# Kernel optimization log

Hardware: AMD Instinct MI355X
Metric: run time of the kernel (lower is better)

The kernel has to match this reference:

```python
import jax, jax.numpy as jnp
import numpy as np


def setup_inputs() -> dict:
    key = jax.random.key(0)
    k1, k2 = jax.random.split(key)
    input_tensor = jax.random.normal(k1, (32, 128, 64, 64), dtype=jnp.float32)
    weights = jax.random.normal(k2, (256, 128, 3, 3), dtype=jnp.float32) * 0.05
    return {"input_tensor": input_tensor, "weights": weights}


def reference(input_tensor, weights):
    # Valid-padding, stride-1, no-bias direct conv2d (NCHW x OIHW -> NCHW),
    # identical math to the quintuple-loop slice*weight sum in the original.
    return jax.lax.conv_general_dilated(
        input_tensor,
        weights,
        window_strides=(1, 1),
        padding="VALID",
        dimension_numbers=("NCHW", "OIHW", "NCHW"),
    )
```

## Files before the change

kernel.cpp:

```cpp
#include <hip/hip_runtime.h>
#include <hip/hip_bf16.h>

#define N_IMG 32
#define CIN   128
#define INH   64
#define INW   64
#define COUT  256
#define OH    62
#define OW    62

#define IN_BLOCKS 2048
#define WT_BLOCKS (294912 / 256)

typedef short          bf16x8 __attribute__((ext_vector_type(8)));
typedef unsigned short u16x8  __attribute__((ext_vector_type(8)));
typedef float          f32x4  __attribute__((ext_vector_type(4)));
typedef float          f32x2  __attribute__((ext_vector_type(2)));

__device__ __forceinline__ unsigned short f2bf(float x) {
    unsigned int u = __float_as_uint(x);
    u += 0x7fffu + ((u >> 16) & 1u);
    return (unsigned short)(u >> 16);
}

__device__ __forceinline__ void gload_lds16(const void* g, void* l) {
    __builtin_amdgcn_global_load_lds(
        (const __attribute__((address_space(1))) unsigned int*)g,
        (__attribute__((address_space(3))) unsigned int*)l, 16, 0, 0);
}

__global__ __launch_bounds__(256)
void transform_kernel(const float* __restrict__ In,
                      const float* __restrict__ Wsrc,
                      unsigned short* __restrict__ TIn,
                      unsigned short* __restrict__ WT) {
    if (blockIdx.x >= IN_BLOCKS) {
        int idx = (blockIdx.x - IN_BLOCKS) * 256 + threadIdx.x;
        int i   = idx & 7;
        int co  = (idx >> 3) & 255;
        int cgk = idx >> 11;
        int cg  = cgk & 15;
        int khw = cgk >> 4;
        int kh  = khw / 3, kw = khw - 3 * kh;
        int ci  = cg * 8 + i;
        WT[idx] = f2bf(Wsrc[co * (CIN * 9) + ci * 9 + kh * 3 + kw]);
        return;
    }
    __shared__ float T[32][66];
    const int bid = blockIdx.x;
    const int ih0 = (bid & 15) * 4;
    const int cb  = (bid >> 4) & 3;
    const int img = bid >> 6;

    const int r   = threadIdx.x >> 3;
    const int c0  = (threadIdx.x & 7) * 8;
    const int c   = threadIdx.x;
    const int iw  = c >> 2;
    const int cg  = (c & 3) ^ ((iw >> 1) & 3);

    for (int j = 0; j < 4; ++j) {
        const int ih = ih0 + j;
        const float* p = In + (((size_t)(img * CIN + cb * 32 + r)) * INH + ih) * INW + c0;
        f32x4 a = *(const f32x4*)p;
        f32x4 b = *(const f32x4*)(p + 4);
        *(f32x2*)&T[r][c0 + 0] = f32x2{a[0], a[1]};
        *(f32x2*)&T[r][c0 + 2] = f32x2{a[2], a[3]};
        *(f32x2*)&T[r][c0 + 4] = f32x2{b[0], b[1]};
        *(f32x2*)&T[r][c0 + 6] = f32x2{b[2], b[3]};
        __syncthreads();
        u16x8 v;
#pragma unroll
        for (int i = 0; i < 8; ++i) v[i] = f2bf(T[cg * 8 + i][iw]);
        *(u16x8*)&TIn[((size_t)((img * 4 + cb) * 64 + ih) * 256 + c) * 8] = v;
        if (j < 3) __syncthreads();
    }
}

__global__ __launch_bounds__(256, 4)
void conv_mfma_bf16_kernel(const unsigned short* __restrict__ TIn,
                           const unsigned short* __restrict__ WT,
                           float* __restrict__ Out) {
    __shared__ unsigned short Lin[2][2112];

    const int g   = blockIdx.x;
    const int f   = (g & 7) * 248 + (g >> 3);
    const int img = f / OH;
    const int oh  = f - img * OH;

    const int tid  = threadIdx.x;
    const int wave = tid >> 6;
    const int lane = tid & 63;
    const int q    = lane >> 4;
    const int ml   = lane & 15;
    const int co_base = wave * 64;

    const unsigned short* tin_base = TIn + (size_t)img * (4 * 64 * 2048);
    const bf16x8* WTv = (const bf16x8*)WT;
    const int wlane = q * 256 + co_base + ml;

    int xoff[3][4];
#pragma unroll
    for (int kw = 0; kw < 3; ++kw)
#pragma unroll
        for (int ni = 0; ni < 4; ++ni) {
            const int r = ni * 16 + ml + kw;
            xoff[kw][ni] = r * 32 + ((q ^ ((r >> 1) & 3)) << 3);
        }

    f32x4 acc[4][4];
    const f32x4 zero = {0.f, 0.f, 0.f, 0.f};
#pragma unroll
    for (int a = 0; a < 4; ++a)
#pragma unroll
        for (int b = 0; b < 4; ++b) acc[a][b] = zero;

    gload_lds16(tin_base + oh * 2048 + tid * 8, &Lin[0][wave * 512]);
    if (tid < 64) ((unsigned int*)&Lin[tid >> 5][64 * 32])[tid & 31] = 0u;
    __syncthreads();

#pragma unroll
    for (int s = 0; s < 12; ++s) {
        const int cur = s & 1;
        const int kh = s >> 2, cb = s & 3;
        const bf16x8* wstage = WTv + (kh * 3 * 16 + cb * 4) * 256;

        bf16x8 wA[4], wB[4];
#pragma unroll
        for (int mi = 0; mi < 4; ++mi) wA[mi] = wstage[wlane + mi * 16];
#pragma unroll
        for (int mi = 0; mi < 4; ++mi) wB[mi] = wstage[4096 + wlane + mi * 16];

        if (s < 11) {
            const int s1 = s + 1;
            const unsigned short* src =
                tin_base + ((s1 & 3) * 64 + oh + (s1 >> 2)) * 2048;
            gload_lds16(src + tid * 8, &Lin[cur ^ 1][wave * 512]);
        }

        {
            bf16x8 xf[4];
#pragma unroll
            for (int ni = 0; ni < 4; ++ni)
                xf[ni] = *(const bf16x8*)&Lin[cur][xoff[0][ni]];
#pragma unroll
            for (int mi = 0; mi < 4; ++mi)
#pragma unroll
                for (int ni = 0; ni < 4; ++ni)
                    acc[mi][ni] = __builtin_amdgcn_mfma_f32_16x16x32_bf16(
                        wA[mi], xf[ni], acc[mi][ni], 0, 0, 0);
        }
#pragma unroll
        for (int mi = 0; mi < 4; ++mi) wA[mi] = wstage[2 * 4096 + wlane + mi * 16];
        {
            bf16x8 xf[4];
#pragma unroll
            for (int ni = 0; ni < 4; ++ni)
                xf[ni] = *(const bf16x8*)&Lin[cur][xoff[1][ni]];
#pragma unroll
            for (int mi = 0; mi < 4; ++mi)
#pragma unroll
                for (int ni = 0; ni < 4; ++ni)
                    acc[mi][ni] = __builtin_amdgcn_mfma_f32_16x16x32_bf16(
                        wB[mi], xf[ni], acc[mi][ni], 0, 0, 0);
        }
        {
            bf16x8 xf[4];
#pragma unroll
            for (int ni = 0; ni < 4; ++ni)
                xf[ni] = *(const bf16x8*)&Lin[cur][xoff[2][ni]];
#pragma unroll
            for (int mi = 0; mi < 4; ++mi)
#pragma unroll
                for (int ni = 0; ni < 4; ++ni)
                    acc[mi][ni] = __builtin_amdgcn_mfma_f32_16x16x32_bf16(
                        wA[mi], xf[ni], acc[mi][ni], 0, 0, 0);
        }
        __syncthreads();
    }

#pragma unroll
    for (int mi = 0; mi < 4; ++mi) {
#pragma unroll
        for (int r = 0; r < 4; ++r) {
            const int co = co_base + mi * 16 + q * 4 + r;
            float* op = Out + ((img * COUT + co) * OH + oh) * OW;
#pragma unroll
            for (int ni = 0; ni < 4; ++ni) {
                const int ow = ni * 16 + ml;
                if (ow < OW) op[ow] = acc[mi][ni][r];
            }
        }
    }
}

__global__ void wt_transform_kernel(const float* __restrict__ Wsrc,
                                    unsigned short* __restrict__ WT) {
    int idx = blockIdx.x * 256 + threadIdx.x;
    int i   = idx & 7;
    int co  = (idx >> 3) & 255;
    int cgk = idx >> 11;
    int cg  = cgk & 15;
    int khw = cgk >> 4;
    int kh  = khw / 3, kw = khw - 3 * kh;
    int ci  = cg * 8 + i;
    WT[idx] = f2bf(Wsrc[co * (CIN * 9) + ci * 9 + kh * 3 + kw]);
}

__global__ __launch_bounds__(256, 2)
void conv_mfma_fp32_kernel(const float* __restrict__ In,
                           const unsigned short* __restrict__ WT,
                           float* __restrict__ Out) {
    __shared__ unsigned short Lin[66 * 32];

    const int oh   = blockIdx.x;
    const int img  = blockIdx.y;
    const int tid  = threadIdx.x;
    const int wave = tid >> 6;
    const int lane = tid & 63;
    const int q    = lane >> 4;
    const int ml   = lane & 15;
    const int co_base = wave * 64;

    f32x4 acc[4][4];
    const f32x4 zero = {0.f, 0.f, 0.f, 0.f};
#pragma unroll
    for (int a = 0; a < 4; ++a)
#pragma unroll
        for (int b = 0; b < 4; ++b) acc[a][b] = zero;

    if (tid < 32) ((unsigned int*)&Lin[64 * 32])[tid] = 0u;

    const int s_iw = tid & 63;
    const int s_cg = tid >> 6;
    const bf16x8* WTv = (const bf16x8*)WT;

    for (int kh = 0; kh < 3; ++kh) {
        const int ih = oh + kh;
        for (int cb = 0; cb < 4; ++cb) {
            const float* p = In + (((img * CIN + cb * 32 + s_cg * 8) * INH + ih) * INW + s_iw);
            u16x8 v;
#pragma unroll
            for (int i = 0; i < 8; ++i) v[i] = f2bf(p[i * (INH * INW)]);
            __syncthreads();
            *(u16x8*)&Lin[s_iw * 32 + ((s_cg ^ (s_iw & 3)) << 3)] = v;
            __syncthreads();

#pragma unroll
            for (int kw = 0; kw < 3; ++kw) {
                const int khw = kh * 3 + kw;
                bf16x8 wf[4], xf[4];
#pragma unroll
                for (int mi = 0; mi < 4; ++mi)
                    wf[mi] = WTv[(khw * 16 + cb * 4 + q) * 256 + co_base + mi * 16 + ml];
#pragma unroll
                for (int ni = 0; ni < 4; ++ni) {
                    const int row = ni * 16 + ml + kw;
                    xf[ni] = *(const bf16x8*)&Lin[row * 32 + ((q ^ (row & 3)) << 3)];
                }
#pragma unroll
                for (int mi = 0; mi < 4; ++mi)
#pragma unroll
                    for (int ni = 0; ni < 4; ++ni)
                        acc[mi][ni] = __builtin_amdgcn_mfma_f32_16x16x32_bf16(
                            wf[mi], xf[ni], acc[mi][ni], 0, 0, 0);
            }
        }
    }

#pragma unroll
    for (int mi = 0; mi < 4; ++mi) {
#pragma unroll
        for (int r = 0; r < 4; ++r) {
            const int co = co_base + mi * 16 + q * 4 + r;
            float* op = Out + ((img * COUT + co) * OH + oh) * OW;
#pragma unroll
            for (int ni = 0; ni < 4; ++ni) {
                const int ow = ni * 16 + ml;
                if (ow < OW) op[ow] = acc[mi][ni][r];
            }
        }
    }
}

__global__ void conv_naive_kernel(const float* __restrict__ In,
                                  const float* __restrict__ Wt,
                                  float* __restrict__ Out) {
    int idx = blockIdx.x * 256 + threadIdx.x;
    const int total = N_IMG * COUT * OH * OW;
    if (idx >= total) return;
    int ow = idx % OW; int t = idx / OW;
    int oh = t % OH;   t /= OH;
    int co = t % COUT; int img = t / COUT;
    float s = 0.f;
    for (int ci = 0; ci < CIN; ++ci)
#pragma unroll
        for (int kh = 0; kh < 3; ++kh)
#pragma unroll
            for (int kw = 0; kw < 3; ++kw)
                s += In[((img * CIN + ci) * INH + oh + kh) * INW + ow + kw] *
                     Wt[co * CIN * 9 + ci * 9 + kh * 3 + kw];
    Out[idx] = s;
}

extern "C" void kernel_launch(void* const* d_in, const int* in_sizes, int n_in,
                              void* d_out, int out_size, void* d_ws, size_t ws_size,
                              hipStream_t stream) {
    const float* In   = (const float*)d_in[0];
    const float* Wsrc = (const float*)d_in[1];
    float* Out        = (float*)d_out;

    const size_t WT_BYTES  = (size_t)9 * 16 * 256 * 8 * sizeof(unsigned short);
    const size_t TIN_BYTES = (size_t)N_IMG * 4 * 64 * 2048 * sizeof(unsigned short);

    if (ws_size >= WT_BYTES + TIN_BYTES) {
        unsigned short* WT  = (unsigned short*)d_ws;
        unsigned short* TIn = (unsigned short*)((char*)d_ws + WT_BYTES);
        transform_kernel<<<dim3(IN_BLOCKS + WT_BLOCKS), dim3(256), 0, stream>>>(In, Wsrc, TIn, WT);
        conv_mfma_bf16_kernel<<<dim3(OH * N_IMG), dim3(256), 0, stream>>>(TIn, WT, Out);
    } else if (ws_size >= WT_BYTES) {
        unsigned short* WT = (unsigned short*)d_ws;
        wt_transform_kernel<<<dim3(WT_BLOCKS), dim3(256), 0, stream>>>(Wsrc, WT);
        conv_mfma_fp32_kernel<<<dim3(OH, N_IMG), dim3(256), 0, stream>>>(In, WT, Out);
    } else {
        const int total = N_IMG * COUT * OH * OW;
        conv_naive_kernel<<<dim3((total + 255) / 256), dim3(256), 0, stream>>>(In, Wsrc, Out);
    }
}
```

Baseline: 239.6 us.

## Give each wave a private input LDS buffer and drop per-stage block barriers

```diff
diff --git a/kernel.cpp b/kernel.cpp
--- a/kernel.cpp
+++ b/kernel.cpp
@@ -80,7 +80,7 @@
 void conv_mfma_bf16_kernel(const unsigned short* __restrict__ TIn,
                            const unsigned short* __restrict__ WT,
                            float* __restrict__ Out) {
-    __shared__ unsigned short Lin[2][2112];
+    __shared__ unsigned short Lin[4][2][2112];
 
     const int g   = blockIdx.x;
     const int f   = (g & 7) * 248 + (g >> 3);
@@ -114,68 +114,80 @@
 #pragma unroll
         for (int b = 0; b < 4; ++b) acc[a][b] = zero;
 
-    gload_lds16(tin_base + oh * 2048 + tid * 8, &Lin[0][wave * 512]);
-    if (tid < 64) ((unsigned int*)&Lin[tid >> 5][64 * 32])[tid & 31] = 0u;
+    ((unsigned int*)&Lin[wave][lane >> 5][2048])[lane & 31] = 0u;
+    {
+        const unsigned short* row0 = tin_base + oh * 2048;
+#pragma unroll
+        for (int k = 0; k < 4; ++k)
+            gload_lds16(row0 + k * 512 + lane * 8, &Lin[wave][0][k * 512]);
+    }
     __syncthreads();
 
 #pragma unroll
     for (int s = 0; s < 12; ++s) {
         const int cur = s & 1;
         const int kh = s >> 2, cb = s & 3;
-        const bf16x8* wstage = WTv + (kh * 3 * 16 + cb * 4) * 256;
-
-        bf16x8 wA[4], wB[4];
-#pragma unroll
-        for (int mi = 0; mi < 4; ++mi) wA[mi] = wstage[wlane + mi * 16];
-#pragma unroll
-        for (int mi = 0; mi < 4; ++mi) wB[mi] = wstage[4096 + wlane + mi * 16];
+        const bf16x8* wstage = WTv + (kh * 48 + cb * 4) * 256;
+
+        bf16x8 w0[4], w1[4], w2[4];
+#pragma unroll
+        for (int mi = 0; mi < 4; ++mi) w0[mi] = wstage[wlane + mi * 16];
+
+        asm volatile("s_waitcnt vmcnt(4)" ::: "memory");
+
+#pragma unroll
+        for (int mi = 0; mi < 4; ++mi) w1[mi] = wstage[4096 + wlane + mi * 16];
+
+        {
+            bf16x8 xf[4];
+#pragma unroll
+            for (int ni = 0; ni < 4; ++ni)
+                xf[ni] = *(const bf16x8*)&Lin[wave][cur][xoff[0][ni]];
+#pragma unroll
+            for (int mi = 0; mi < 4; ++mi)
+#pragma unroll
+                for (int ni = 0; ni < 4; ++ni)
+                    acc[mi][ni] = __builtin_amdgcn_mfma_f32_16x16x32_bf16(
+                        w0[mi], xf[ni], acc[mi][ni], 0, 0, 0);
+        }
+#pragma unroll
+        for (int mi = 0; mi < 4; ++mi) w2[mi] = wstage[8192 + wlane + mi * 16];
 
         if (s < 11) {
+            __builtin_amdgcn_sched_barrier(0);
             const int s1 = s + 1;
             const unsigned short* src =
                 tin_base + ((s1 & 3) * 64 + oh + (s1 >> 2)) * 2048;
-            gload_lds16(src + tid * 8, &Lin[cur ^ 1][wave * 512]);
+#pragma unroll
+            for (int k = 0; k < 4; ++k)
+                gload_lds16(src + k * 512 + lane * 8, &Lin[wave][cur ^ 1][k * 512]);
+            __builtin_amdgcn_sched_barrier(0);
         }
 
         {
             bf16x8 xf[4];
 #pragma unroll
             for (int ni = 0; ni < 4; ++ni)
-                xf[ni] = *(const bf16x8*)&Lin[cur][xoff[0][ni]];
+                xf[ni] = *(const bf16x8*)&Lin[wave][cur][xoff[1][ni]];
 #pragma unroll
             for (int mi = 0; mi < 4; ++mi)
 #pragma unroll
                 for (int ni = 0; ni < 4; ++ni)
                     acc[mi][ni] = __builtin_amdgcn_mfma_f32_16x16x32_bf16(
-                        wA[mi], xf[ni], acc[mi][ni], 0, 0, 0);
-        }
-#pragma unroll
-        for (int mi = 0; mi < 4; ++mi) wA[mi] = wstage[2 * 4096 + wlane + mi * 16];
+                        w1[mi], xf[ni], acc[mi][ni], 0, 0, 0);
+        }
         {
             bf16x8 xf[4];
 #pragma unroll
             for (int ni = 0; ni < 4; ++ni)
-                xf[ni] = *(const bf16x8*)&Lin[cur][xoff[1][ni]];
+                xf[ni] = *(const bf16x8*)&Lin[wave][cur][xoff[2][ni]];
 #pragma unroll
             for (int mi = 0; mi < 4; ++mi)
 #pragma unroll
                 for (int ni = 0; ni < 4; ++ni)
                     acc[mi][ni] = __builtin_amdgcn_mfma_f32_16x16x32_bf16(
-                        wB[mi], xf[ni], acc[mi][ni], 0, 0, 0);
-        }
-        {
-            bf16x8 xf[4];
-#pragma unroll
-            for (int ni = 0; ni < 4; ++ni)
-                xf[ni] = *(const bf16x8*)&Lin[cur][xoff[2][ni]];
-#pragma unroll
-            for (int mi = 0; mi < 4; ++mi)
-#pragma unroll
-                for (int ni = 0; ni < 4; ++ni)
-                    acc[mi][ni] = __builtin_amdgcn_mfma_f32_16x16x32_bf16(
-                        wA[mi], xf[ni], acc[mi][ni], 0, 0, 0);
-        }
-        __syncthreads();
+                        w2[mi], xf[ni], acc[mi][ni], 0, 0, 0);
+        }
     }
 
 #pragma unroll
```

Result: slower. 277.0 us (+15.6%).
